# Kernel optimization log

Measured on AMD Instinct MI355X. Metric: run time of the kernel, lower is better.

## Reference

```python
import jax, jax.numpy as jnp
import numpy as np

SIGMA = 1.0

def setup_inputs() -> dict:
    key = jax.random.key(0)
    k1, k2, k3 = jax.random.split(key, 3)
    X_new = jax.random.normal(k1, (8192, 128), dtype=jnp.float32)
    X_train = jax.random.normal(k2, (32768, 128), dtype=jnp.float32)
    atomic_weights = jax.random.normal(k3, (32768, 1), dtype=jnp.float32)
    return {"X_new": X_new, "X_train": X_train, "atomic_weights": atomic_weights}

def reference(X_new, X_train, atomic_weights):
    x2 = jnp.sum(X_new * X_new, axis=-1, keepdims=True)            # [N_new, 1]
    y2 = jnp.sum(X_train * X_train, axis=-1)                       # [N_train]
    cross = jnp.einsum('nd,md->nm', X_new, X_train)                # [N_new, N_train]
    dist_sq = jnp.maximum(x2 + y2[None, :] - 2.0 * cross, 0.0)
    K_new = jnp.exp(-dist_sq / (2.0 * SIGMA ** 2))
    per_atom_energy = K_new @ atomic_weights                       # [N_new, 1]
    return per_atom_energy
```

## Files before the change

kernel.cpp:

```cpp
#include <hip/hip_runtime.h>
#include <stdint.h>

typedef __attribute__((ext_vector_type(4))) int i32x4;
typedef __attribute__((ext_vector_type(16))) int i32x16;
typedef __attribute__((ext_vector_type(8))) short short8;
typedef __attribute__((ext_vector_type(16))) float f32x16;

#define LOG2E 1.4426950408889634f
#define S1 16.0f
#define S1_INV 0.0625f
#define S2 4096.0f
#define K2 (1.0f / 65536.0f)

__device__ inline float fast_exp2(float x) {
#if __has_builtin(__builtin_amdgcn_exp2f)
  return __builtin_amdgcn_exp2f(x);
#else
  float r;
  asm("v_exp_f32 %0, %1" : "=v"(r) : "v"(x));
  return r;
#endif
}

__device__ inline void gload16(const void* g, void* l) {
  __builtin_amdgcn_global_load_lds(
      (const __attribute__((address_space(1))) void*)g,
      (__attribute__((address_space(3))) void*)l, 16, 0, 0);
}
__device__ inline void gload4(const void* g, void* l) {
  __builtin_amdgcn_global_load_lds(
      (const __attribute__((address_space(1))) void*)g,
      (__attribute__((address_space(3))) void*)l, 4, 0, 0);
}

__device__ inline void q4(float4 v, float pre, int& hw, int& lw) {
  float xs[4] = {v.x, v.y, v.z, v.w};
  int h = 0, l = 0;
#pragma unroll
  for (int j = 0; j < 4; ++j) {
    float x = xs[j] * pre;
    float hf = rintf(fminf(fmaxf(x * S1, -127.f), 127.f));
    float rf = x - hf * S1_INV;
    float lf = rintf(fminf(fmaxf(rf * S2, -127.f), 127.f));
    h |= ((int)hf & 255) << (8 * j);
    l |= ((int)lf & 255) << (8 * j);
  }
  hw = h;
  lw = l;
}

__global__ __launch_bounds__(256) void gk_conv_s(const float* __restrict__ Xtr,
                                                 const float* __restrict__ wts,
                                                 char* __restrict__ planes,
                                                 float* __restrict__ s, int M) {
  int g = blockIdx.x * 256 + threadIdx.x;
  int row = g >> 3;
  int gr = g & 7;
  if (row >= M) return;
  const float* p = Xtr + (size_t)row * 128 + gr * 16;
  int hw[4], lw[4];
  float ss = 0.f;
#pragma unroll
  for (int i = 0; i < 4; ++i) {
    float4 v = *(const float4*)(p + i * 4);
    ss += v.x * v.x + v.y * v.y + v.z * v.z + v.w * v.w;
    q4(v, 1.0f, hw[i], lw[i]);
  }
  ss += __shfl_xor(ss, 1, 64);
  ss += __shfl_xor(ss, 2, 64);
  ss += __shfl_xor(ss, 4, 64);
  if (gr == 0) s[row] = expf(-0.5f * ss) * wts[row];

  int T = row >> 5, r = row & 31;
  size_t base = (size_t)T * 8192 + (gr >> 1) * 1024 + (gr & 1) * 512 + r * 16;
  *(i32x4*)(planes + base) = (i32x4){hw[0], hw[1], hw[2], hw[3]};
  *(i32x4*)(planes + base + 4096) = (i32x4){lw[0], lw[1], lw[2], lw[3]};
}

__global__ __launch_bounds__(256, 4) void gk_main_i8(
    const float* __restrict__ Xnew, const char* __restrict__ planes,
    const float* __restrict__ s, float* __restrict__ out, int N, int M,
    int mchunk) {
  extern __shared__ char dlds[];

  const int t = threadIdx.x;
  const int l = t & 63;
  const int w = t >> 6;
  const int cl = l & 31;
  const int lk = l >> 5;

  const int n0 = blockIdx.x * 128;
  const int M0 = blockIdx.y * mchunk;
  const int iters = mchunk >> 5;
  const int T0 = M0 >> 5;

#define ZERO16 ((i32x16){0, 0, 0, 0, 0, 0, 0, 0, 0, 0, 0, 0, 0, 0, 0, 0})

#define STAGE(tt)                                                       \
  {                                                                     \
    int st_ = ((tt) < iters) ? (tt) : (iters - 1);   \
    const char* src_ = planes + (size_t)(T0 + st_) * 8192 + t * 16;     \
    char* dst_ = dlds + ((tt)&3) * 8192 + t * 16;                       \
    gload16(src_, dst_);                                                \
    gload16(src_ + 4096, dst_ + 4096);                                  \
    gload4(s + M0 + st_ * 32 + l, dlds + 32768 + ((tt)&3) * 256);       \
  }

#define MFMAS(acc_hh, acc_m, tile)                                      \
  {                                                                     \
    const char* buf_ = dlds + ((tile)&3) * 8192;                        \
    _Pragma("unroll") for (int kf = 0; kf < 4; ++kf) {                  \
      const char* kb_ = buf_ + kf * 1024 + lk * 512 + cl * 16;          \
      i32x4 ah_ = *(const i32x4*)(kb_);                                 \
      i32x4 al_ = *(const i32x4*)(kb_ + 4096);                          \
      acc_hh = __builtin_amdgcn_mfma_i32_32x32x32_i8(ah_, bh[kf], acc_hh, 0, 0, 0); \
      acc_m = __builtin_amdgcn_mfma_i32_32x32x32_i8(ah_, bl[kf], acc_m, 0, 0, 0);   \
      acc_m = __builtin_amdgcn_mfma_i32_32x32x32_i8(al_, bh[kf], acc_m, 0, 0, 0);   \
    }                                                                   \
  }

#define EPI_RAW(acc_hh, acc_m, tile)                                    \
  {                                                                     \
    const float4* sl4_ =                                                \
        (const float4*)(dlds + 32768 + ((tile)&3) * 256);               \
    _Pragma("unroll") for (int q = 0; q < 4; ++q) {                     \
      float4 sv_ = sl4_[q * 2 + lk];                                    \
      _Pragma("unroll") for (int j = 0; j < 4; ++j) {                   \
        int r_ = q * 4 + j;                                             \
        float c_ = (float)((acc_hh[r_] << 8) + acc_m[r_]) * K2;         \
        out0 += fast_exp2(c_) * (&sv_.x)[j];                            \
      }                                                                 \
    }                                                                   \
  }

#define FUSED(accC_hh, accC_m, tileC, accP_hh, accP_m, tileP)           \
  {                                                                     \
    const char* buf_ = dlds + ((tileC)&3) * 8192;                       \
    const float4* sl4_ =                                                \
        (const float4*)(dlds + 32768 + ((tileP)&3) * 256);              \
    _Pragma("unroll") for (int kf = 0; kf < 4; ++kf) {                  \
      const char* kb_ = buf_ + kf * 1024 + lk * 512 + cl * 16;          \
      i32x4 ah_ = *(const i32x4*)(kb_);                                 \
      i32x4 al_ = *(const i32x4*)(kb_ + 4096);                          \
      accC_hh = __builtin_amdgcn_mfma_i32_32x32x32_i8(ah_, bh[kf], accC_hh, 0, 0, 0); \
      accC_m = __builtin_amdgcn_mfma_i32_32x32x32_i8(ah_, bl[kf], accC_m, 0, 0, 0);   \
      accC_m = __builtin_amdgcn_mfma_i32_32x32x32_i8(al_, bh[kf], accC_m, 0, 0, 0);   \
      float4 sv_ = sl4_[kf * 2 + lk];                                   \
      _Pragma("unroll") for (int j = 0; j < 4; ++j) {                   \
        int r_ = kf * 4 + j;                                            \
        float c_ = (float)((accP_hh[r_] << 8) + accP_m[r_]) * K2;       \
        out0 += fast_exp2(c_) * (&sv_.x)[j];                            \
      }                                                                 \
    }                                                                   \
    accP_hh = ZERO16;                                                   \
    accP_m = ZERO16;                                                    \
  }

#define REGION_END                                                      \
  asm volatile("s_waitcnt vmcnt(3)" ::: "memory");                      \
  __builtin_amdgcn_s_barrier();

  STAGE(0);
  STAGE(1);

  i32x4 bh[4], bl[4];
  float pref;
  {
    float ss = 0.f;
    const float* pc = Xnew + (size_t)(n0 + w * 32 + cl) * 128;
#pragma unroll
    for (int kf = 0; kf < 4; ++kf) {
      const float* p = pc + kf * 32 + lk * 16;
      int hw[4], lw[4];
#pragma unroll
      for (int i = 0; i < 4; ++i) {
        float4 v = *(const float4*)(p + i * 4);
        ss += v.x * v.x + v.y * v.y + v.z * v.z + v.w * v.w;
        q4(v, LOG2E, hw[i], lw[i]);
      }
      bh[kf] = (i32x4){hw[0], hw[1], hw[2], hw[3]};
      bl[kf] = (i32x4){lw[0], lw[1], lw[2], lw[3]};
    }
    ss += __shfl_xor(ss, 32, 64);
    pref = expf(-0.5f * ss);
  }

  float out0 = 0.f;
  i32x16 hhA = ZERO16, mA = ZERO16, hhB = ZERO16, mB = ZERO16;

  asm volatile("s_waitcnt vmcnt(3)" ::: "memory");
  __builtin_amdgcn_s_barrier();

  __builtin_amdgcn_sched_barrier(0);
  STAGE(2);
  MFMAS(hhA, mA, 0);
  REGION_END;

#pragma unroll 1
  for (int tt = 1; tt < iters - 1; tt += 2) {
    __builtin_amdgcn_sched_barrier(0);
    STAGE(tt + 2);
    FUSED(hhB, mB, tt, hhA, mA, tt - 1);
    REGION_END;

    __builtin_amdgcn_sched_barrier(0);
    STAGE(tt + 3);
    FUSED(hhA, mA, tt + 1, hhB, mB, tt);
    REGION_END;
  }

  __builtin_amdgcn_sched_barrier(0);
  FUSED(hhB, mB, iters - 1, hhA, mA, iters - 2);
  EPI_RAW(hhB, mB, iters - 1);

  out0 += __shfl_xor(out0, 32, 64);
  if (l < 32) {
    int n = n0 + w * 32 + l;
    atomicAdd(out + n, pref * out0);
  }
#undef STAGE
#undef MFMAS
#undef EPI_RAW
#undef FUSED
#undef REGION_END
#undef ZERO16
}

__global__ __launch_bounds__(256) void gk_prep(
    const float* __restrict__ Xnew, const float* __restrict__ Xtr,
    const float* __restrict__ w, float* __restrict__ s,
    float* __restrict__ pref, int M, int N) {
  int row = blockIdx.x * 4 + (threadIdx.x >> 6);
  int lane = threadIdx.x & 63;
  if (row >= M + N) return;
  const float* src =
      (row < M) ? (Xtr + (size_t)row * 128) : (Xnew + (size_t)(row - M) * 128);
  float2 v = *(const float2*)(src + lane * 2);
  float ss = v.x * v.x + v.y * v.y;
#pragma unroll
  for (int o = 32; o >= 1; o >>= 1) ss += __shfl_xor(ss, o, 64);
  if (lane == 0) {
    float e = expf(-0.5f * ss);
    if (row < M)
      s[row] = e * w[row];
    else
      pref[row - M] = e;
  }
}

__device__ inline unsigned swz_fb(unsigned off) {
  return off ^ (((off >> 8) & 7u) << 4);
}
__device__ inline void split8(float x0, float x1, float x2, float x3,
                              float x4, float x5, float x6, float x7,
                              float scale, short8& hi, short8& lo) {
  float xs[8] = {x0, x1, x2, x3, x4, x5, x6, x7};
#pragma unroll
  for (int i = 0; i < 8; ++i) {
    float v = xs[i] * scale;
    unsigned u = __float_as_uint(v);
    float hf = __uint_as_float(u & 0xffff0000u);
    float rr = v - hf;
    hi[i] = (short)(u >> 16);
    lo[i] = (short)(__float_as_uint(rr) >> 16);
  }
}

__global__ __launch_bounds__(256, 2) void gk_main_fb(
    const float* __restrict__ Xnew, const float* __restrict__ Xtr,
    const float* __restrict__ s, const float* __restrict__ pref,
    float* __restrict__ out, int N, int M, int mchunk) {
  __shared__ __attribute__((aligned(16))) char lds[33024];
  const int t = threadIdx.x;
  const int l = t & 63;
  const int w = t >> 6;
  const int lrow = l & 31;
  const int lk = l >> 5;
  const int n0 = blockIdx.x * 256;
  const int M0 = blockIdx.y * mchunk;
  const int iters = mchunk >> 6;

  short8 bh[2][8], bl[2][8];
  {
    const int colbase = n0 + w * 64;
#pragma unroll
    for (int nf = 0; nf < 2; ++nf) {
      int col = colbase + nf * 32 + lrow;
      const float* p = Xnew + (size_t)col * 128 + lk * 8;
#pragma unroll
      for (int kf = 0; kf < 8; ++kf) {
        float4 f0 = *(const float4*)(p + kf * 16);
        float4 f1 = *(const float4*)(p + kf * 16 + 4);
        split8(f0.x, f0.y, f0.z, f0.w, f1.x, f1.y, f1.z, f1.w, LOG2E,
               bh[nf][kf], bl[nf][kf]);
      }
    }
  }

  float out0 = 0.f, out1 = 0.f;
  float4 ga[4][2];
  float sreg = 0.f;
  {
    const float* abase = Xtr + (size_t)M0 * 128;
#pragma unroll
    for (int j = 0; j < 4; ++j) {
      int c = t + j * 256;
      int row = c >> 4, oct = c & 15;
      const float* p = abase + (size_t)row * 128 + oct * 8;
      ga[j][0] = *(const float4*)p;
      ga[j][1] = *(const float4*)(p + 4);
    }
    if (t < 64) sreg = s[M0 + t];
  }

#pragma unroll 1
  for (int it = 0; it < iters; ++it) {
    __syncthreads();
#pragma unroll
    for (int j = 0; j < 4; ++j) {
      int c = t + j * 256;
      int row = c >> 4, oct = c & 15;
      unsigned off = swz_fb((unsigned)(row * 256 + oct * 16));
      short8 hi, lo;
      split8(ga[j][0].x, ga[j][0].y, ga[j][0].z, ga[j][0].w, ga[j][1].x,
             ga[j][1].y, ga[j][1].z, ga[j][1].w, 1.0f, hi, lo);
      *(short8*)(lds + off) = hi;
      *(short8*)(lds + 16384 + off) = lo;
    }
    if (t < 64) *(float*)(lds + 32768 + t * 4) = sreg;
    __syncthreads();
    if (it + 1 < iters) {
      const float* abase = Xtr + (size_t)(M0 + (it + 1) * 64) * 128;
#pragma unroll
      for (int j = 0; j < 4; ++j) {
        int c = t + j * 256;
        int row = c >> 4, oct = c & 15;
        const float* p = abase + (size_t)row * 128 + oct * 8;
        ga[j][0] = *(const float4*)p;
        ga[j][1] = *(const float4*)(p + 4);
      }
      if (t < 64) sreg = s[M0 + (it + 1) * 64 + t];
    }
#pragma unroll
    for (int mf = 0; mf < 2; ++mf) {
      f32x16 acc0 = {0, 0, 0, 0, 0, 0, 0, 0, 0, 0, 0, 0, 0, 0, 0, 0};
      f32x16 acc1 = {0, 0, 0, 0, 0, 0, 0, 0, 0, 0, 0, 0, 0, 0, 0, 0};
#pragma unroll
      for (int kf = 0; kf < 8; ++kf) {
        unsigned off =
            swz_fb((unsigned)((mf * 32 + lrow) * 256 + kf * 32 + lk * 16));
        short8 ah = *(const short8*)(lds + off);
        short8 al = *(const short8*)(lds + 16384 + off);
        acc0 = __builtin_amdgcn_mfma_f32_32x32x16_bf16(ah, bh[0][kf], acc0, 0, 0, 0);
        acc1 = __builtin_amdgcn_mfma_f32_32x32x16_bf16(ah, bh[1][kf], acc1, 0, 0, 0);
        acc0 = __builtin_amdgcn_mfma_f32_32x32x16_bf16(ah, bl[0][kf], acc0, 0, 0, 0);
        acc1 = __builtin_amdgcn_mfma_f32_32x32x16_bf16(ah, bl[1][kf], acc1, 0, 0, 0);
        acc0 = __builtin_amdgcn_mfma_f32_32x32x16_bf16(al, bh[0][kf], acc0, 0, 0, 0);
        acc1 = __builtin_amdgcn_mfma_f32_32x32x16_bf16(al, bh[1][kf], acc1, 0, 0, 0);
      }
      const float* sl = (const float*)(lds + 32768 + mf * 128);
#pragma unroll
      for (int r = 0; r < 16; ++r) {
        int row = (r & 3) + 8 * (r >> 2) + 4 * lk;
        float sv = sl[row];
        out0 += fast_exp2(acc0[r]) * sv;
        out1 += fast_exp2(acc1[r]) * sv;
      }
    }
  }
  out0 += __shfl_xor(out0, 32, 64);
  out1 += __shfl_xor(out1, 32, 64);
  if (l < 32) {
    int n = n0 + w * 64 + l;
    atomicAdd(out + n, pref[n] * out0);
    n += 32;
    atomicAdd(out + n, pref[n] * out1);
  }
}

extern "C" void kernel_launch(void* const* d_in, const int* in_sizes, int n_in,
                              void* d_out, int out_size, void* d_ws,
                              size_t ws_size, hipStream_t stream) {
  const float* Xnew = (const float*)d_in[0];
  const float* Xtr = (const float*)d_in[1];
  const float* wts = (const float*)d_in[2];
  float* out = (float*)d_out;

  const int N = in_sizes[0] / 128;
  const int M = in_sizes[1] / 128;

  char* ws = (char*)d_ws;
  float* s_ws = (float*)ws;
  char* planes_ws = ws + (size_t)M * 4;
  const size_t need = (size_t)M * 4 + (size_t)M * 256;

  hipMemsetAsync(d_out, 0, (size_t)N * sizeof(float), stream);

  if (ws_size >= need) {
    gk_conv_s<<<dim3(M * 8 / 256), 256, 0, stream>>>(Xtr, wts, planes_ws,
                                                     s_ws, M);
    const int SPLIT = 16;
    dim3 grid(N / 128, SPLIT);
    gk_main_i8<<<grid, 256, 33792, stream>>>(Xnew, planes_ws, s_ws, out, N, M,
                                             M / SPLIT);
  } else {
    float* pref_ws = s_ws + M;
    int rows = M + N;
    gk_prep<<<dim3((rows + 3) / 4), 256, 0, stream>>>(Xnew, Xtr, wts, s_ws,
                                                      pref_ws, M, N);
    const int SPLIT = 16;
    dim3 grid(N / 256, SPLIT);
    gk_main_fb<<<grid, 256, 0, stream>>>(Xnew, Xtr, s_ws, pref_ws, out, N, M,
                                         M / SPLIT);
  }
}
```

Baseline: 127.8 us.

## Replace ping-pong MFMA/epilogue software pipeline with single-accumulator loop

Removes the two-accumulator software pipeline that overlapped the MFMAs for one tile with the exp epilogue of the previous tile. Each iteration now runs the MFMAs for a tile and then its epilogue on one accumulator pair. The first MFMA takes a zero constant as input instead of explicitly re-zeroing the accumulators. This halves accumulator register use, which may help occupancy or register pressure, but it gives up overlap between the matrix units and the exp/VALU work, since the epilogue now depends directly on the MFMA results just produced.

```diff
diff --git a/kernel.cpp b/kernel.cpp
--- a/kernel.cpp
+++ b/kernel.cpp
@@ -94,8 +94,6 @@
   const int iters = mchunk >> 5;
   const int T0 = M0 >> 5;
 
-#define ZERO16 ((i32x16){0, 0, 0, 0, 0, 0, 0, 0, 0, 0, 0, 0, 0, 0, 0, 0})
-
 #define STAGE(tt)                                                       \
   {                                                                     \
     int st_ = ((tt) < iters) ? (tt) : (iters - 1);   \
@@ -106,10 +104,18 @@
     gload4(s + M0 + st_ * 32 + l, dlds + 32768 + ((tt)&3) * 256);       \
   }
 
-#define MFMAS(acc_hh, acc_m, tile)                                      \
+#define MFMAS_Z(acc_hh, acc_m, tile)                                    \
   {                                                                     \
     const char* buf_ = dlds + ((tile)&3) * 8192;                        \
-    _Pragma("unroll") for (int kf = 0; kf < 4; ++kf) {                  \
+    {                                                                   \
+      const char* kb_ = buf_ + lk * 512 + cl * 16;                      \
+      i32x4 ah_ = *(const i32x4*)(kb_);                                 \
+      i32x4 al_ = *(const i32x4*)(kb_ + 4096);                          \
+      acc_hh = __builtin_amdgcn_mfma_i32_32x32x32_i8(ah_, bh[0], zc, 0, 0, 0);      \
+      acc_m = __builtin_amdgcn_mfma_i32_32x32x32_i8(ah_, bl[0], zc, 0, 0, 0);       \
+      acc_m = __builtin_amdgcn_mfma_i32_32x32x32_i8(al_, bh[0], acc_m, 0, 0, 0);    \
+    }                                                                   \
+    _Pragma("unroll") for (int kf = 1; kf < 4; ++kf) {                  \
       const char* kb_ = buf_ + kf * 1024 + lk * 512 + cl * 16;          \
       i32x4 ah_ = *(const i32x4*)(kb_);                                 \
       i32x4 al_ = *(const i32x4*)(kb_ + 4096);                          \
@@ -119,7 +125,7 @@
     }                                                                   \
   }
 
-#define EPI_RAW(acc_hh, acc_m, tile)                                    \
+#define EPI(acc_hh, acc_m, tile)                                        \
   {                                                                     \
     const float4* sl4_ =                                                \
         (const float4*)(dlds + 32768 + ((tile)&3) * 256);               \
@@ -133,29 +139,6 @@
     }                                                                   \
   }
 
-#define FUSED(accC_hh, accC_m, tileC, accP_hh, accP_m, tileP)           \
-  {                                                                     \
-    const char* buf_ = dlds + ((tileC)&3) * 8192;                       \
-    const float4* sl4_ =                                                \
-        (const float4*)(dlds + 32768 + ((tileP)&3) * 256);              \
-    _Pragma("unroll") for (int kf = 0; kf < 4; ++kf) {                  \
-      const char* kb_ = buf_ + kf * 1024 + lk * 512 + cl * 16;          \
-      i32x4 ah_ = *(const i32x4*)(kb_);                                 \
-      i32x4 al_ = *(const i32x4*)(kb_ + 4096);                          \
-      accC_hh = __builtin_amdgcn_mfma_i32_32x32x32_i8(ah_, bh[kf], accC_hh, 0, 0, 0); \
-      accC_m = __builtin_amdgcn_mfma_i32_32x32x32_i8(ah_, bl[kf], accC_m, 0, 0, 0);   \
-      accC_m = __builtin_amdgcn_mfma_i32_32x32x32_i8(al_, bh[kf], accC_m, 0, 0, 0);   \
-      float4 sv_ = sl4_[kf * 2 + lk];                                   \
-      _Pragma("unroll") for (int j = 0; j < 4; ++j) {                   \
-        int r_ = kf * 4 + j;                                            \
-        float c_ = (float)((accP_hh[r_] << 8) + accP_m[r_]) * K2;       \
-        out0 += fast_exp2(c_) * (&sv_.x)[j];                            \
-      }                                                                 \
-    }                                                                   \
-    accP_hh = ZERO16;                                                   \
-    accP_m = ZERO16;                                                    \
-  }
-
 #define REGION_END                                                      \
   asm volatile("s_waitcnt vmcnt(3)" ::: "memory");                      \
   __builtin_amdgcn_s_barrier();
@@ -186,32 +169,20 @@
   }
 
   float out0 = 0.f;
-  i32x16 hhA = ZERO16, mA = ZERO16, hhB = ZERO16, mB = ZERO16;
+  const i32x16 zc = {0, 0, 0, 0, 0, 0, 0, 0, 0, 0, 0, 0, 0, 0, 0, 0};
+  i32x16 hh, m;
 
   asm volatile("s_waitcnt vmcnt(3)" ::: "memory");
   __builtin_amdgcn_s_barrier();
 
-  __builtin_amdgcn_sched_barrier(0);
-  STAGE(2);
-  MFMAS(hhA, mA, 0);
-  REGION_END;
-
 #pragma unroll 1
-  for (int tt = 1; tt < iters - 1; tt += 2) {
+  for (int it = 0; it < iters; ++it) {
     __builtin_amdgcn_sched_barrier(0);
-    STAGE(tt + 2);
-    FUSED(hhB, mB, tt, hhA, mA, tt - 1);
+    STAGE(it + 2);
+    MFMAS_Z(hh, m, it);
+    EPI(hh, m, it);
     REGION_END;
-
-    __builtin_amdgcn_sched_barrier(0);
-    STAGE(tt + 3);
-    FUSED(hhA, mA, tt + 1, hhB, mB, tt);
-    REGION_END;
-  }
-
-  __builtin_amdgcn_sched_barrier(0);
-  FUSED(hhB, mB, iters - 1, hhA, mA, iters - 2);
-  EPI_RAW(hhB, mB, iters - 1);
+  }
 
   out0 += __shfl_xor(out0, 32, 64);
   if (l < 32) {
@@ -219,11 +190,9 @@
     atomicAdd(out + n, pref * out0);
   }
 #undef STAGE
-#undef MFMAS
-#undef EPI_RAW
-#undef FUSED
+#undef MFMAS_Z
+#undef EPI
 #undef REGION_END
-#undef ZERO16
 }
 
 __global__ __launch_bounds__(256) void gk_prep(
```

Measured after the change: 131.4 us. 2.8% more time.
